# Performance work log

Measured on AMD Instinct MI355X. Metric: run time of the kernel, lower is better.

The kernel has to match this reference:

```python
import jax, jax.numpy as jnp
import numpy as np

T, B, D, H, R, S, M = 1024, 16, 512, 8, 32, 16, 16
TQ = R + T + S   # query length
KL = M + R + T   # key/value length
NEG_INF = -1e8


def setup_inputs() -> dict:
    key = jax.random.key(0)
    ks = jax.random.split(key, 12)
    utterance = jax.random.normal(ks[0], (T, B, D), jnp.float32)
    right_context = jax.random.normal(ks[1], (R, B, D), jnp.float32)
    summary = jax.random.normal(ks[2], (S, B, D), jnp.float32)
    mems = jax.random.normal(ks[3], (M, B, D), jnp.float32)
    # valid lengths in [T//2, T]; force max == T so data-dependent shapes are static
    lengths = jax.random.randint(ks[4], (B,), T // 2, T + 1).at[0].set(T).astype(jnp.int64)
    # block-streaming style mask: query i may only attend to keys <= i + M
    q_idx = jnp.arange(TQ)[:, None]
    k_idx = jnp.arange(KL)[None, :]
    attention_mask = k_idx > (q_idx + M)  # True = masked
    scale = 0.02
    Wq = jax.random.normal(ks[5], (D, D), jnp.float32) * scale
    bq = jnp.zeros((D,), jnp.float32)
    Wkv = jax.random.normal(ks[6], (2 * D, D), jnp.float32) * scale
    bkv = jnp.zeros((2 * D,), jnp.float32)
    Wo = jax.random.normal(ks[7], (D, D), jnp.float32) * scale
    bo = jnp.zeros((D,), jnp.float32)
    return dict(utterance=utterance, lengths=lengths, right_context=right_context,
                summary=summary, mems=mems, attention_mask=attention_mask,
                Wq=Wq, bq=bq, Wkv=Wkv, bkv=bkv, Wo=Wo, bo=bo)


def _split_heads(x):
    # (L, B, D) -> (B*H, L, D//H), matching torch .view(-1, B*H, d).transpose(0, 1)
    L = x.shape[0]
    return x.reshape(L, B * H, D // H).transpose(1, 0, 2)


def reference(utterance, lengths, right_context, summary, mems, attention_mask,
              Wq, bq, Wkv, bkv, Wo, bo):
    d_head = D // H
    scaling = d_head ** -0.5

    query_in = jnp.concatenate([right_context, utterance, summary], axis=0)   # (TQ, B, D)
    kv_in = jnp.concatenate([mems, right_context, utterance], axis=0)         # (KL, B, D)

    query = query_in @ Wq.T + bq
    kv = kv_in @ Wkv.T + bkv
    k, v = jnp.split(kv, 2, axis=2)

    q = _split_heads(query)  # (B*H, TQ, d)
    kh = _split_heads(k)     # (B*H, KL, d)
    vh = _split_heads(v)

    w = jnp.einsum('nqd,nkd->nqk', q * scaling, kh).astype(jnp.float32)
    w = jnp.where(attention_mask[None, :, :], NEG_INF, w)

    # padding mask (B > 1 path): klengths = lengths + M + right_context_blocks_length
    rcbl = TQ - jnp.max(lengths) - S  # == R since max(lengths) == T
    klengths = lengths + M + rcbl
    pad_mask = jnp.arange(KL)[None, :] >= klengths[:, None]  # (B, KL)
    w = w.reshape(B, H, TQ, KL)
    w = jnp.where(pad_mask[:, None, None, :], NEG_INF, w)
    w = w.reshape(B * H, TQ, KL)

    probs = jax.nn.softmax(w, axis=-1)  # dropout p=0.0
    attn = jnp.einsum('nqk,nkd->nqd', probs, vh)          # (B*H, TQ, d)
    attn = attn.transpose(1, 0, 2).reshape(TQ, B, D)

    out = attn @ Wo.T + bo                                # (TQ, B, D)
    output_right_context = out[:TQ - S]                    # (R+T, B, D)
    output_mems = jnp.clip(out[TQ - S:], -10.0, 10.0)      # tanh_on_mem=False
    return output_right_context, output_mems[:-1]          # (S-1, B, D)
```

## Files before the change

### kernel.cpp

```cpp
#include <hip/hip_runtime.h>

#define T_   1024
#define B_   16
#define D_   512
#define H_   8
#define R_   32
#define S_   16
#define M_   16
#define TQ_  1072
#define KL_  1072
#define DH_  64
#define NROW 17152
#define K_   512
#define QSCALE 0.18033688f

typedef unsigned short u16;
using bf16x8 = __attribute__((ext_vector_type(8))) short;
using f32x4  = __attribute__((ext_vector_type(4))) float;
using u16x4  = __attribute__((ext_vector_type(4))) unsigned short;

__device__ __forceinline__ u16 f2bf(float f) {
    unsigned int u = __builtin_bit_cast(unsigned int, f);
    unsigned int r = u + 0x7fffu + ((u >> 16) & 1u);
    return (u16)(r >> 16);
}

__device__ __forceinline__ void gload_lds16(const u16* g, u16* l) {
    __builtin_amdgcn_global_load_lds(
        (const __attribute__((address_space(1))) unsigned int*)g,
        (__attribute__((address_space(3))) unsigned int*)l,
        16, 0, 0);
}

__global__ void k_convert4(const float4* __restrict__ utt, const float4* __restrict__ rc,
                           const float4* __restrict__ smr, const float4* __restrict__ mems,
                           const float4* __restrict__ Wq, const float4* __restrict__ Wkv,
                           const float4* __restrict__ Wo,
                           u16x4* __restrict__ xq, u16x4* __restrict__ xkv,
                           u16x4* __restrict__ wq, u16x4* __restrict__ wkv,
                           u16x4* __restrict__ wo)
{
    const int N4 = NROW * D_ / 4;
    const int RB = R_ * B_ * D_ / 4, TB = (R_ + T_) * B_ * D_ / 4;
    const int MB = M_ * B_ * D_ / 4, MRB = (M_ + R_) * B_ * D_ / 4;
    const int W1 = D_ * D_ / 4, W2 = 2 * D_ * D_ / 4;
    for (int i = blockIdx.x * blockDim.x + threadIdx.x; i < N4;
         i += gridDim.x * blockDim.x) {
        float4 v;
        if (i < RB)      v = rc[i];
        else if (i < TB) v = utt[i - RB];
        else             v = smr[i - TB];
        xq[i] = (u16x4){f2bf(v.x), f2bf(v.y), f2bf(v.z), f2bf(v.w)};
        if (i < MB)       v = mems[i];
        else if (i < MRB) v = rc[i - MB];
        else              v = utt[i - MRB];
        xkv[i] = (u16x4){f2bf(v.x), f2bf(v.y), f2bf(v.z), f2bf(v.w)};
        if (i < W1) { v = Wq[i]; wq[i] = (u16x4){f2bf(v.x), f2bf(v.y), f2bf(v.z), f2bf(v.w)}; }
        if (i < W2) { v = Wkv[i]; wkv[i] = (u16x4){f2bf(v.x), f2bf(v.y), f2bf(v.z), f2bf(v.w)}; }
        if (i < W1) { v = Wo[i]; wo[i] = (u16x4){f2bf(v.x), f2bf(v.y), f2bf(v.z), f2bf(v.w)}; }
    }
}

__global__ __launch_bounds__(256, 2)
void k_gemm_qkv(const u16* __restrict__ xq, const u16* __restrict__ xkv,
                const u16* __restrict__ wqp, const u16* __restrict__ wkvp,
                const float* __restrict__ bq, const float* __restrict__ bkv,
                u16* __restrict__ qb, u16* __restrict__ kb, u16* __restrict__ vt)
{
    __shared__ __align__(16) u16 As[128 * 32];
    __shared__ __align__(16) u16 Bs[128 * 32];

    const int tm = blockIdx.x;
    const int tn = blockIdx.y;
    const bool isQ = tn < 4;
    const int wr0 = (isQ ? tn : tn - 4) * 128;
    const u16* A = isQ ? xq : xkv;
    const u16* W = (isQ ? wqp : wkvp) + (size_t)wr0 * K_;
    const float* bias = isQ ? bq : bkv;

    const int w    = threadIdx.x >> 6;
    const int lane = threadIdx.x & 63;
    const int wm = w >> 1, wn = w & 1;
    const int col = lane & 15, quad = lane >> 4;

    const int srow = lane >> 2;
    const int skof = (lane & 3) * 8;
    const u16* gA = A + (size_t)(tm * 128 + w * 32 + srow) * K_ + skof;
    const u16* gW = W + (size_t)(w * 32 + srow) * K_ + skof;
    u16* lA = &As[(w * 32) * 32];
    u16* lB = &Bs[(w * 32) * 32];

    f32x4 acc[4][4];
#pragma unroll
    for (int mi = 0; mi < 4; mi++)
#pragma unroll
        for (int ni = 0; ni < 4; ni++) acc[mi][ni] = (f32x4){0.f, 0.f, 0.f, 0.f};

    for (int k0 = 0; k0 < K_; k0 += 32) {
        __syncthreads();
        gload_lds16(gA + k0,            lA);
        gload_lds16(gA + k0 + 16 * K_,  lA + 16 * 32);
        gload_lds16(gW + k0,            lB);
        gload_lds16(gW + k0 + 16 * K_,  lB + 16 * 32);
        __syncthreads();

        bf16x8 aF[4], bF[4];
#pragma unroll
        for (int mi = 0; mi < 4; mi++)
            aF[mi] = *(const bf16x8*)&As[(wm * 64 + mi * 16 + col) * 32 + quad * 8];
#pragma unroll
        for (int ni = 0; ni < 4; ni++)
            bF[ni] = *(const bf16x8*)&Bs[(wn * 64 + ni * 16 + col) * 32 + quad * 8];
#pragma unroll
        for (int mi = 0; mi < 4; mi++)
#pragma unroll
            for (int ni = 0; ni < 4; ni++)
                acc[mi][ni] = __builtin_amdgcn_mfma_f32_16x16x32_bf16(
                                  aF[mi], bF[ni], acc[mi][ni], 0, 0, 0);
    }

#pragma unroll
    for (int ni = 0; ni < 4; ni++) {
        int gcol = wr0 + wn * 64 + ni * 16 + col;
        float bs = bias[gcol];
        if (!isQ && gcol >= 512) {
            int f  = gcol - 512;
            int l0 = tm * 8 + wm * 4;
#pragma unroll
            for (int r = 0; r < 4; r++) {
                int bb = quad * 4 + r;
                u16x4 pk;
#pragma unroll
                for (int mi = 0; mi < 4; mi++)
                    pk[mi] = f2bf(acc[mi][ni][r] + bs);
                *(u16x4*)&vt[((size_t)(bb * 512 + f)) * KL_ + l0] = pk;
            }
            continue;
        }
#pragma unroll
        for (int mi = 0; mi < 4; mi++) {
#pragma unroll
            for (int r = 0; r < 4; r++) {
                int mrow = tm * 128 + wm * 64 + mi * 16 + quad * 4 + r;
                float val = acc[mi][ni][r] + bs;
                if (isQ) qb[(size_t)mrow * 512 + gcol] = f2bf(val * QSCALE);
                else     kb[(size_t)mrow * 512 + gcol] = f2bf(val);
            }
        }
    }
}

__global__ __launch_bounds__(256, 2)
void k_gemm_o(const u16* __restrict__ A, const u16* __restrict__ W,
              const float* __restrict__ bias, float* __restrict__ Co)
{
    __shared__ __align__(16) u16 As[128 * 32];
    __shared__ __align__(16) u16 Bs[128 * 32];

    const int tm = blockIdx.x;
    const int tn = blockIdx.y;
    const int w    = threadIdx.x >> 6;
    const int lane = threadIdx.x & 63;
    const int wm = w >> 1, wn = w & 1;
    const int col = lane & 15, quad = lane >> 4;

    const int srow = lane >> 2;
    const int skof = (lane & 3) * 8;
    const u16* gA = A + (size_t)(tm * 128 + w * 32 + srow) * K_ + skof;
    const u16* gW = W + (size_t)(tn * 128 + w * 32 + srow) * K_ + skof;
    u16* lA = &As[(w * 32) * 32];
    u16* lB = &Bs[(w * 32) * 32];

    f32x4 acc[4][4];
#pragma unroll
    for (int mi = 0; mi < 4; mi++)
#pragma unroll
        for (int ni = 0; ni < 4; ni++) acc[mi][ni] = (f32x4){0.f, 0.f, 0.f, 0.f};

    for (int k0 = 0; k0 < K_; k0 += 32) {
        __syncthreads();
        gload_lds16(gA + k0,            lA);
        gload_lds16(gA + k0 + 16 * K_,  lA + 16 * 32);
        gload_lds16(gW + k0,            lB);
        gload_lds16(gW + k0 + 16 * K_,  lB + 16 * 32);
        __syncthreads();

        bf16x8 aF[4], bF[4];
#pragma unroll
        for (int mi = 0; mi < 4; mi++)
            aF[mi] = *(const bf16x8*)&As[(wm * 64 + mi * 16 + col) * 32 + quad * 8];
#pragma unroll
        for (int ni = 0; ni < 4; ni++)
            bF[ni] = *(const bf16x8*)&Bs[(wn * 64 + ni * 16 + col) * 32 + quad * 8];
#pragma unroll
        for (int mi = 0; mi < 4; mi++)
#pragma unroll
            for (int ni = 0; ni < 4; ni++)
                acc[mi][ni] = __builtin_amdgcn_mfma_f32_16x16x32_bf16(
                                  aF[mi], bF[ni], acc[mi][ni], 0, 0, 0);
    }

#pragma unroll
    for (int ni = 0; ni < 4; ni++) {
        int gcol = tn * 128 + wn * 64 + ni * 16 + col;
        float bs = bias[gcol];
#pragma unroll
        for (int mi = 0; mi < 4; mi++) {
#pragma unroll
            for (int r = 0; r < 4; r++) {
                int mrow = tm * 128 + wm * 64 + mi * 16 + quad * 4 + r;
                int l = mrow >> 4;
                if (l == TQ_ - 1) continue;
                float val = acc[mi][ni][r] + bs;
                if (l >= TQ_ - S_) val = fminf(10.0f, fmaxf(-10.0f, val));
                Co[(size_t)mrow * 512 + gcol] = val;
            }
        }
    }
}

__global__ __launch_bounds__(256, 2)
void k_attn3(const u16* __restrict__ qbuf, const u16* __restrict__ kb,
             const u16* __restrict__ vt, const int* __restrict__ lenp,
             u16* __restrict__ attnb)
{
    __shared__ __align__(16) u16 Ks[2][64 * 64];
    __shared__ __align__(16) u16 Vs[2][64 * 64];
    __shared__ __align__(16) u16 Ps[4][16 * 64];

    const int blk  = blockIdx.x;
    const int qblk = 16 - (blk >> 7);
    const int bh   = blk & 127;
    const int b = bh >> 3, h = bh & 7;
    const int tid = threadIdx.x;
    const int w = tid >> 6, lane = tid & 63;
    const int col = lane & 15, quad = lane >> 4;

    int stride = (lenp[1] == 0) ? 2 : 1;
    int maxlen = 0;
    for (int i = 0; i < B_; i++) maxlen = max(maxlen, lenp[i * stride]);
    const int klen = lenp[b * stride] + M_ + (TQ_ - maxlen - S_);

    const int q0 = qblk * 64;
    const int qw = q0 + w * 16;
    const int q  = qw + col;

    int qrow = min(q, TQ_ - 1);
    const u16* qp = qbuf + ((size_t)qrow * B_ + b) * D_ + h * DH_ + quad * 8;
    bf16x8 bq0 = *(const bf16x8*)(qp);
    bf16x8 bq1 = *(const bf16x8*)(qp + 32);

    const int s0 = tid, s1 = tid + 256;
    const u16* kbase = kb + (size_t)b * 512 + h * DH_;
    size_t kof0 = (size_t)(s0 >> 3) * 8192 + (size_t)(((s0 & 7) ^ ((s0 >> 3) & 7)) * 8);
    size_t kof1 = (size_t)(s1 >> 3) * 8192 + (size_t)(((s1 & 7) ^ ((s1 >> 3) & 7)) * 8);
    const u16* vbase = vt + (size_t)(b * 512 + h * DH_) * KL_;
    size_t vof0 = (size_t)(s0 >> 3) * KL_ + (size_t)(((s0 & 7) ^ ((s0 >> 3) & 7)) * 8);
    size_t vof1 = (size_t)(s1 >> 3) * KL_ + (size_t)(((s1 & 7) ^ ((s1 >> 3) & 7)) * 8);

    float mi = -1e30f, li = 0.f;
    f32x4 o[4];
#pragma unroll
    for (int g = 0; g < 4; g++) o[g] = (f32x4){0.f, 0.f, 0.f, 0.f};

    const int nk = min(q0 + 64 + M_, klen);
    const int numkt = (nk + 63) >> 6;
    u16* pw = &Ps[w][0];

    gload_lds16(kbase + kof0, &Ks[0][(size_t)w * 512]);
    gload_lds16(kbase + kof1, &Ks[0][2048 + (size_t)w * 512]);
    gload_lds16(vbase + vof0, &Vs[0][(size_t)w * 512]);
    gload_lds16(vbase + vof1, &Vs[0][2048 + (size_t)w * 512]);

    for (int kt = 0; kt < numkt; kt++) {
        const int kn0 = kt * 64;
        const int cur = kt & 1;
        __syncthreads();
        if (kt + 1 < numkt) {
            const size_t kn1 = (size_t)(kn0 + 64);
            gload_lds16(kbase + kn1 * 8192 + kof0, &Ks[cur ^ 1][(size_t)w * 512]);
            gload_lds16(kbase + kn1 * 8192 + kof1, &Ks[cur ^ 1][2048 + (size_t)w * 512]);
            gload_lds16(vbase + kn1 + vof0, &Vs[cur ^ 1][(size_t)w * 512]);
            gload_lds16(vbase + kn1 + vof1, &Vs[cur ^ 1][2048 + (size_t)w * 512]);
        }

        f32x4 sc[4];
#pragma unroll
        for (int g = 0; g < 4; g++) {
            int key = g * 16 + col;
            bf16x8 a0 = *(const bf16x8*)&Ks[cur][key * 64 + ((quad ^ (key & 7)) * 8)];
            bf16x8 a1 = *(const bf16x8*)&Ks[cur][key * 64 + (((4 + quad) ^ (key & 7)) * 8)];
            f32x4 z = {0.f, 0.f, 0.f, 0.f};
            z = __builtin_amdgcn_mfma_f32_16x16x32_bf16(a0, bq0, z, 0, 0, 0);
            z = __builtin_amdgcn_mfma_f32_16x16x32_bf16(a1, bq1, z, 0, 0, 0);
            sc[g] = z;
        }

        const bool needmask = (kn0 + 63 > qw + M_) || (kn0 + 63 >= klen);
        if (needmask) {
#pragma unroll
            for (int g = 0; g < 4; g++)
#pragma unroll
                for (int r = 0; r < 4; r++) {
                    int key = kn0 + g * 16 + quad * 4 + r;
                    bool valid = (key <= q + M_) && (key < klen);
                    sc[g][r] = valid ? sc[g][r] : -1e8f;
                }
        }
        float mt = -1e30f;
#pragma unroll
        for (int g = 0; g < 4; g++)
#pragma unroll
            for (int r = 0; r < 4; r++) mt = fmaxf(mt, sc[g][r]);
        mt = fmaxf(mt, __shfl_xor(mt, 16));
        mt = fmaxf(mt, __shfl_xor(mt, 32));
        float mnew  = fmaxf(mi, mt);
        float alpha = __builtin_amdgcn_exp2f(mi - mnew);
        float sum = 0.f;
#pragma unroll
        for (int g = 0; g < 4; g++) {
            u16x4 pk;
#pragma unroll
            for (int r = 0; r < 4; r++) {
                float p = __builtin_amdgcn_exp2f(sc[g][r] - mnew);
                sum += p;
                pk[r] = f2bf(p);
            }
            int kc = g * 2 + (quad >> 1);
            *(u16x4*)&pw[col * 64 + ((kc ^ (col & 7)) * 8) + (quad & 1) * 4] = pk;
        }
        sum += __shfl_xor(sum, 16);
        sum += __shfl_xor(sum, 32);
        li = li * alpha + sum;
        mi = mnew;

#pragma unroll
        for (int r = 0; r < 4; r++) {
            float ar = __shfl(alpha, quad * 4 + r, 16);
#pragma unroll
            for (int g = 0; g < 4; g++) o[g][r] *= ar;
        }

        bf16x8 ap0 = *(const bf16x8*)&pw[col * 64 + ((quad ^ (col & 7)) * 8)];
        bf16x8 ap1 = *(const bf16x8*)&pw[col * 64 + (((4 + quad) ^ (col & 7)) * 8)];
#pragma unroll
        for (int g = 0; g < 4; g++) {
            int d = g * 16 + col;
            bf16x8 bv0 = *(const bf16x8*)&Vs[cur][d * 64 + ((quad ^ (d & 7)) * 8)];
            bf16x8 bv1 = *(const bf16x8*)&Vs[cur][d * 64 + (((4 + quad) ^ (d & 7)) * 8)];
            o[g] = __builtin_amdgcn_mfma_f32_16x16x32_bf16(ap0, bv0, o[g], 0, 0, 0);
            o[g] = __builtin_amdgcn_mfma_f32_16x16x32_bf16(ap1, bv1, o[g], 0, 0, 0);
        }
    }

#pragma unroll
    for (int r = 0; r < 4; r++) {
        float lr = __shfl(li, quad * 4 + r, 16);
        float inv = 1.0f / lr;
        int qo = qw + quad * 4 + r;
        if (qo < TQ_) {
#pragma unroll
            for (int g = 0; g < 4; g++) {
                int d = h * DH_ + g * 16 + col;
                attnb[((size_t)qo * B_ + b) * D_ + d] = f2bf(o[g][r] * inv);
            }
        }
    }
}

extern "C" void kernel_launch(void* const* d_in, const int* in_sizes, int n_in,
                              void* d_out, int out_size, void* d_ws, size_t ws_size,
                              hipStream_t stream)
{
    const float* utt  = (const float*)d_in[0];
    const int*   len  = (const int*)  d_in[1];
    const float* rc   = (const float*)d_in[2];
    const float* smr  = (const float*)d_in[3];
    const float* mems = (const float*)d_in[4];
    const float* Wq   = (const float*)d_in[6];
    const float* bq   = (const float*)d_in[7];
    const float* Wkv  = (const float*)d_in[8];
    const float* bkv  = (const float*)d_in[9];
    const float* Wo   = (const float*)d_in[10];
    const float* bo   = (const float*)d_in[11];

    char* ws = (char*)d_ws;
    size_t off = 0;
    auto alloc = [&](size_t bytes) -> void* {
        void* p = ws + off;
        off += (bytes + 255) & ~(size_t)255;
        return p;
    };
    u16* xq   = (u16*)alloc((size_t)NROW * D_ * 2);
    u16* xkv  = (u16*)alloc((size_t)NROW * D_ * 2);
    u16* wq   = (u16*)alloc((size_t)D_ * D_ * 2);
    u16* wkv  = (u16*)alloc((size_t)2 * D_ * D_ * 2);
    u16* wo   = (u16*)alloc((size_t)D_ * D_ * 2);
    u16* qb   = (u16*)alloc((size_t)NROW * D_ * 2);
    u16* kb   = (u16*)alloc((size_t)NROW * D_ * 2);
    u16* vt   = (u16*)alloc((size_t)B_ * D_ * KL_ * 2 + 512);
    u16* attnb = xq;

    k_convert4<<<2048, 256, 0, stream>>>((const float4*)utt, (const float4*)rc,
                                         (const float4*)smr, (const float4*)mems,
                                         (const float4*)Wq, (const float4*)Wkv,
                                         (const float4*)Wo,
                                         (u16x4*)xq, (u16x4*)xkv,
                                         (u16x4*)wq, (u16x4*)wkv, (u16x4*)wo);
    dim3 gqkv(134, 12);
    k_gemm_qkv<<<gqkv, 256, 0, stream>>>(xq, xkv, wq, wkv, bq, bkv, qb, kb, vt);
    k_attn3<<<17 * 128, 256, 0, stream>>>(qb, kb, vt, len, attnb);
    dim3 go(134, 4);
    k_gemm_o<<<go, 256, 0, stream>>>(attnb, wo, bo, (float*)d_out);
}
```

Before: 248.6 us.

## Share one bf16 input buffer, retile V layout, and swizzle GEMM block order

The query and KV inputs are merged into one bf16 buffer (mems|rc|utt|summary), so Q reads at an offset instead of converting a second copy, which roughly halves conversion writes. The V-transpose output moves to a 4-key-interleaved, XOR-swizzled layout that the GEMM epilogue writes as contiguous chunks, and the attention kernel reassembles the B operands from paired 8-byte LDS reads. Both GEMMs switch to a 1D grid with grouped tile ordering so nearby blocks share A and W tiles in cache. The cost is more complex indexing in the attention inner loop, extra LDS reads per MFMA operand, and wasted blocks that exit early in the padded grid.

After: 219.4 us. 1.13x faster.

```diff
diff --git a/kernel.cpp b/kernel.cpp
--- a/kernel.cpp
+++ b/kernel.cpp
@@ -12,6 +12,7 @@
 #define DH_  64
 #define NROW 17152
 #define K_   512
+#define LQ_  268
 #define QSCALE 0.18033688f
 
 typedef unsigned short u16;
@@ -36,45 +37,46 @@
                            const float4* __restrict__ smr, const float4* __restrict__ mems,
                            const float4* __restrict__ Wq, const float4* __restrict__ Wkv,
                            const float4* __restrict__ Wo,
-                           u16x4* __restrict__ xq, u16x4* __restrict__ xkv,
+                           u16x4* __restrict__ xall,
                            u16x4* __restrict__ wq, u16x4* __restrict__ wkv,
                            u16x4* __restrict__ wo)
 {
-    const int N4 = NROW * D_ / 4;
-    const int RB = R_ * B_ * D_ / 4, TB = (R_ + T_) * B_ * D_ / 4;
-    const int MB = M_ * B_ * D_ / 4, MRB = (M_ + R_) * B_ * D_ / 4;
+    const int N4 = 17408 * D_ / 4;
+    const int MB = M_ * B_ * D_ / 4;
+    const int RB = MB + R_ * B_ * D_ / 4;
+    const int UB = RB + T_ * B_ * D_ / 4;
     const int W1 = D_ * D_ / 4, W2 = 2 * D_ * D_ / 4;
     for (int i = blockIdx.x * blockDim.x + threadIdx.x; i < N4;
          i += gridDim.x * blockDim.x) {
         float4 v;
-        if (i < RB)      v = rc[i];
-        else if (i < TB) v = utt[i - RB];
-        else             v = smr[i - TB];
-        xq[i] = (u16x4){f2bf(v.x), f2bf(v.y), f2bf(v.z), f2bf(v.w)};
-        if (i < MB)       v = mems[i];
-        else if (i < MRB) v = rc[i - MB];
-        else              v = utt[i - MRB];
-        xkv[i] = (u16x4){f2bf(v.x), f2bf(v.y), f2bf(v.z), f2bf(v.w)};
-        if (i < W1) { v = Wq[i]; wq[i] = (u16x4){f2bf(v.x), f2bf(v.y), f2bf(v.z), f2bf(v.w)}; }
+        if (i < MB)      v = mems[i];
+        else if (i < RB) v = rc[i - MB];
+        else if (i < UB) v = utt[i - RB];
+        else             v = smr[i - UB];
+        xall[i] = (u16x4){f2bf(v.x), f2bf(v.y), f2bf(v.z), f2bf(v.w)};
+        if (i < W1) { v = Wq[i];  wq[i]  = (u16x4){f2bf(v.x), f2bf(v.y), f2bf(v.z), f2bf(v.w)}; }
         if (i < W2) { v = Wkv[i]; wkv[i] = (u16x4){f2bf(v.x), f2bf(v.y), f2bf(v.z), f2bf(v.w)}; }
-        if (i < W1) { v = Wo[i]; wo[i] = (u16x4){f2bf(v.x), f2bf(v.y), f2bf(v.z), f2bf(v.w)}; }
+        if (i < W1) { v = Wo[i];  wo[i]  = (u16x4){f2bf(v.x), f2bf(v.y), f2bf(v.z), f2bf(v.w)}; }
     }
 }
 
 __global__ __launch_bounds__(256, 2)
-void k_gemm_qkv(const u16* __restrict__ xq, const u16* __restrict__ xkv,
+void k_gemm_qkv(const u16* __restrict__ xall,
                 const u16* __restrict__ wqp, const u16* __restrict__ wkvp,
                 const float* __restrict__ bq, const float* __restrict__ bkv,
                 u16* __restrict__ qb, u16* __restrict__ kb, u16* __restrict__ vt)
 {
+    const int bid = blockIdx.x;
+    const int tn = (bid % 96) >> 3;
+    const int tm = (bid / 96) * 8 + (bid & 7);
+    if (tm >= 134) return;
+
     __shared__ __align__(16) u16 As[128 * 32];
     __shared__ __align__(16) u16 Bs[128 * 32];
 
-    const int tm = blockIdx.x;
-    const int tn = blockIdx.y;
     const bool isQ = tn < 4;
     const int wr0 = (isQ ? tn : tn - 4) * 128;
-    const u16* A = isQ ? xq : xkv;
+    const u16* A = isQ ? (xall + (size_t)256 * K_) : xall;
     const u16* W = (isQ ? wqp : wkvp) + (size_t)wr0 * K_;
     const float* bias = isQ ? bq : bkv;
 
@@ -125,7 +127,7 @@
         float bs = bias[gcol];
         if (!isQ && gcol >= 512) {
             int f  = gcol - 512;
-            int l0 = tm * 8 + wm * 4;
+            int lq = tm * 2 + wm;
 #pragma unroll
             for (int r = 0; r < 4; r++) {
                 int bb = quad * 4 + r;
@@ -133,7 +135,7 @@
 #pragma unroll
                 for (int mi = 0; mi < 4; mi++)
                     pk[mi] = f2bf(acc[mi][ni][r] + bs);
-                *(u16x4*)&vt[((size_t)(bb * 512 + f)) * KL_ + l0] = pk;
+                *(u16x4*)&vt[(((size_t)bb * LQ_ + lq) * 512 + f) * 4] = pk;
             }
             continue;
         }
@@ -154,11 +156,14 @@
 void k_gemm_o(const u16* __restrict__ A, const u16* __restrict__ W,
               const float* __restrict__ bias, float* __restrict__ Co)
 {
+    const int bid = blockIdx.x;
+    const int tn = (bid % 32) >> 3;
+    const int tm = (bid / 32) * 8 + (bid & 7);
+    if (tm >= 134) return;
+
     __shared__ __align__(16) u16 As[128 * 32];
     __shared__ __align__(16) u16 Bs[128 * 32];
 
-    const int tm = blockIdx.x;
-    const int tn = blockIdx.y;
     const int w    = threadIdx.x >> 6;
     const int lane = threadIdx.x & 63;
     const int wm = w >> 1, wn = w & 1;
@@ -220,7 +225,7 @@
 }
 
 __global__ __launch_bounds__(256, 2)
-void k_attn3(const u16* __restrict__ qbuf, const u16* __restrict__ kb,
+void k_attn4(const u16* __restrict__ qbuf, const u16* __restrict__ kb,
              const u16* __restrict__ vt, const int* __restrict__ lenp,
              u16* __restrict__ attnb)
 {
@@ -254,9 +259,13 @@
     const u16* kbase = kb + (size_t)b * 512 + h * DH_;
     size_t kof0 = (size_t)(s0 >> 3) * 8192 + (size_t)(((s0 & 7) ^ ((s0 >> 3) & 7)) * 8);
     size_t kof1 = (size_t)(s1 >> 3) * 8192 + (size_t)(((s1 & 7) ^ ((s1 >> 3) & 7)) * 8);
-    const u16* vbase = vt + (size_t)(b * 512 + h * DH_) * KL_;
-    size_t vof0 = (size_t)(s0 >> 3) * KL_ + (size_t)(((s0 & 7) ^ ((s0 >> 3) & 7)) * 8);
-    size_t vof1 = (size_t)(s1 >> 3) * KL_ + (size_t)(((s1 & 7) ^ ((s1 >> 3) & 7)) * 8);
+    const u16* vbase = vt + ((size_t)b * LQ_ * 512 + (size_t)h * DH_) * 4;
+    auto vchunk = [](int s) -> size_t {
+        int fp = s >> 4;
+        int lq = (s & 15) ^ (fp & 15);
+        return (size_t)lq * 2048 + (size_t)fp * 8;
+    };
+    const size_t vof0 = vchunk(s0), vof1 = vchunk(s1);
 
     float mi = -1e30f, li = 0.f;
     f32x4 o[4];
@@ -277,11 +286,12 @@
         const int cur = kt & 1;
         __syncthreads();
         if (kt + 1 < numkt) {
-            const size_t kn1 = (size_t)(kn0 + 64);
-            gload_lds16(kbase + kn1 * 8192 + kof0, &Ks[cur ^ 1][(size_t)w * 512]);
-            gload_lds16(kbase + kn1 * 8192 + kof1, &Ks[cur ^ 1][2048 + (size_t)w * 512]);
-            gload_lds16(vbase + kn1 + vof0, &Vs[cur ^ 1][(size_t)w * 512]);
-            gload_lds16(vbase + kn1 + vof1, &Vs[cur ^ 1][2048 + (size_t)w * 512]);
+            const size_t kstep = (size_t)(kn0 + 64) * 8192;
+            const size_t vstep = (size_t)(kt + 1) * 32768;
+            gload_lds16(kbase + kstep + kof0, &Ks[cur ^ 1][(size_t)w * 512]);
+            gload_lds16(kbase + kstep + kof1, &Ks[cur ^ 1][2048 + (size_t)w * 512]);
+            gload_lds16(vbase + vstep + vof0, &Vs[cur ^ 1][(size_t)w * 512]);
+            gload_lds16(vbase + vstep + vof1, &Vs[cur ^ 1][2048 + (size_t)w * 512]);
         }
 
         f32x4 sc[4];
@@ -346,10 +356,22 @@
 #pragma unroll
         for (int g = 0; g < 4; g++) {
             int d = g * 16 + col;
-            bf16x8 bv0 = *(const bf16x8*)&Vs[cur][d * 64 + ((quad ^ (d & 7)) * 8)];
-            bf16x8 bv1 = *(const bf16x8*)&Vs[cur][d * 64 + (((4 + quad) ^ (d & 7)) * 8)];
-            o[g] = __builtin_amdgcn_mfma_f32_16x16x32_bf16(ap0, bv0, o[g], 0, 0, 0);
-            o[g] = __builtin_amdgcn_mfma_f32_16x16x32_bf16(ap1, bv1, o[g], 0, 0, 0);
+            int fp = d >> 1, fo = (d & 1) * 4;
+            bf16x8 bv[2];
+#pragma unroll
+            for (int hh = 0; hh < 2; hh++) {
+                int lqA = hh * 8 + quad * 2;
+                int posA = fp * 16 + (lqA ^ (fp & 15));
+                int posB = fp * 16 + ((lqA + 1) ^ (fp & 15));
+                u16x4 loA = *(const u16x4*)&Vs[cur][posA * 8 + fo];
+                u16x4 loB = *(const u16x4*)&Vs[cur][posB * 8 + fo];
+                bf16x8 t;
+                t[0] = loA[0]; t[1] = loA[1]; t[2] = loA[2]; t[3] = loA[3];
+                t[4] = loB[0]; t[5] = loB[1]; t[6] = loB[2]; t[7] = loB[3];
+                bv[hh] = t;
+            }
+            o[g] = __builtin_amdgcn_mfma_f32_16x16x32_bf16(ap0, bv[0], o[g], 0, 0, 0);
+            o[g] = __builtin_amdgcn_mfma_f32_16x16x32_bf16(ap1, bv[1], o[g], 0, 0, 0);
         }
     }
 
@@ -391,25 +413,22 @@
         off += (bytes + 255) & ~(size_t)255;
         return p;
     };
-    u16* xq   = (u16*)alloc((size_t)NROW * D_ * 2);
-    u16* xkv  = (u16*)alloc((size_t)NROW * D_ * 2);
+    u16* xall = (u16*)alloc((size_t)17408 * D_ * 2);
     u16* wq   = (u16*)alloc((size_t)D_ * D_ * 2);
     u16* wkv  = (u16*)alloc((size_t)2 * D_ * D_ * 2);
     u16* wo   = (u16*)alloc((size_t)D_ * D_ * 2);
     u16* qb   = (u16*)alloc((size_t)NROW * D_ * 2);
     u16* kb   = (u16*)alloc((size_t)NROW * D_ * 2);
-    u16* vt   = (u16*)alloc((size_t)B_ * D_ * KL_ * 2 + 512);
-    u16* attnb = xq;
+    u16* vt   = (u16*)alloc((size_t)B_ * LQ_ * 512 * 4 * 2 + 65536);
+    u16* attnb = xall;
 
     k_convert4<<<2048, 256, 0, stream>>>((const float4*)utt, (const float4*)rc,
                                          (const float4*)smr, (const float4*)mems,
                                          (const float4*)Wq, (const float4*)Wkv,
                                          (const float4*)Wo,
-                                         (u16x4*)xq, (u16x4*)xkv,
+                                         (u16x4*)xall,
                                          (u16x4*)wq, (u16x4*)wkv, (u16x4*)wo);
-    dim3 gqkv(134, 12);
-    k_gemm_qkv<<<gqkv, 256, 0, stream>>>(xq, xkv, wq, wkv, bq, bkv, qb, kb, vt);
-    k_attn3<<<17 * 128, 256, 0, stream>>>(qb, kb, vt, len, attnb);
-    dim3 go(134, 4);
-    k_gemm_o<<<go, 256, 0, stream>>>(attnb, wo, bo, (float*)d_out);
-}
+    k_gemm_qkv<<<17 * 96, 256, 0, stream>>>(xall, wq, wkv, bq, bkv, qb, kb, vt);
+    k_attn4<<<17 * 128, 256, 0, stream>>>(qb, kb, vt, len, attnb);
+    k_gemm_o<<<17 * 32, 256, 0, stream>>>(attnb, wo, bo, (float*)d_out);
+}
```
